# Performance work log

Measured on AMD Instinct MI355X. Metric: run time of the kernel, lower is better.

## Reference

```python
import jax, jax.numpy as jnp
import numpy as np

N, E = 50000, 800000          # nodes, edges
CUR, HID, OUT = 128, 128, 128  # cur_dim, hidden_dim, output_dim
NEG_SLOPE = 0.01               # F.leaky_relu default


def setup_inputs() -> dict:
    key = jax.random.key(0)
    ks = jax.random.split(key, 12)
    rn = lambda k, shp, s: jax.random.normal(k, shp, dtype=jnp.float32) * s
    s_c, s_h, s_o = 1.0 / np.sqrt(CUR), 1.0 / np.sqrt(HID), 1.0 / np.sqrt(OUT)
    return {
        "h": rn(ks[0], (N, CUR), 1.0),
        "x": rn(ks[1], (N, CUR), 1.0),
        "edge_index": jax.random.randint(ks[2], (2, E), 0, N, dtype=jnp.int32),
        "edge_weight": jax.random.uniform(ks[3], (E,), dtype=jnp.float32),
        # preprocessor_x: Linear(CUR, HID)
        "Wp": rn(ks[4], (HID, CUR), s_c), "bp": jnp.zeros((HID,), jnp.float32),
        # ChebConv(HID, OUT, K=2): two weight mats + bias
        "Wc0": rn(ks[5], (OUT, HID), s_h), "Wc1": rn(ks[6], (OUT, HID), s_h),
        "bc": jnp.zeros((OUT,), jnp.float32),
        # SAGEConv(HID, OUT): lin_rel (neighbors, with bias) + lin_root (self)
        "Wrel": rn(ks[7], (OUT, HID), s_h), "brel": jnp.zeros((OUT,), jnp.float32),
        "Wroot": rn(ks[8], (OUT, HID), s_h),
        # final Linear(OUT, OUT)
        "Wl": rn(ks[9], (OUT, OUT), s_o), "bl": jnp.zeros((OUT,), jnp.float32),
    }


def reference(h, x, edge_index, edge_weight, Wp, bp, Wc0, Wc1, bc,
              Wrel, brel, Wroot, Wl, bl):
    n = x.shape[0]
    src, dst = edge_index[0], edge_index[1]
    seg = lambda d, i: jax.ops.segment_sum(d, i, num_segments=n)

    his = x
    xh = x @ Wp.T + bp                               # [N, HID]

    # --- ChebConv, K=2, sym norm, lambda_max=2 => Lhat = -D^{-1/2} A D^{-1/2}
    deg = seg(edge_weight, src)                       # weighted degree
    dis = jnp.where(deg > 0, jax.lax.rsqrt(jnp.where(deg > 0, deg, 1.0)), 0.0)
    norm = -dis[src] * edge_weight * dis[dst]         # [E]
    Tx1 = seg(norm[:, None] * xh[src], dst)           # [N, HID]
    o1 = jax.nn.leaky_relu(xh @ Wc0.T + Tx1 @ Wc1.T + bc, NEG_SLOPE)

    # --- SAGEConv: mean of edge_weight-scaled neighbor feats + root transform
    msum = seg(edge_weight[:, None] * xh[src], dst)   # [N, HID]
    cnt = seg(jnp.ones_like(edge_weight), dst)        # in-degree
    mean = msum / jnp.maximum(cnt, 1.0)[:, None]
    o2 = jax.nn.leaky_relu(mean @ Wrel.T + brel + xh @ Wroot.T, NEG_SLOPE)

    o3 = (o1 + o2) @ Wl.T + bl
    return (his, o3)
```

## Files before the change

kernel.cpp:

```cpp
#include <hip/hip_runtime.h>

#define NN 50000
#define EE 800000
#define D  128
#define NCH 64
#define CH  12500
#define NR  8
#define RS  6250
#define KCB 512
#define XHB 782
#define CSB 196
#define PKB 384

typedef short short8 __attribute__((ext_vector_type(8)));
typedef float floatx4 __attribute__((ext_vector_type(4)));

__device__ __forceinline__ float leaky(float v) { return v > 0.f ? v : 0.01f * v; }

__device__ __forceinline__ unsigned short f2bf(float f) {
    unsigned int u = __float_as_uint(f);
    u = (u + 0x7fff + ((u >> 16) & 1)) >> 16;
    return (unsigned short)u;
}
__device__ __forceinline__ float bf2f(unsigned int h) {
    return __uint_as_float(h << 16);
}

__global__ __launch_bounds__(256) void k_pre(
    const float* __restrict__ Wp,  const float* __restrict__ Wc0,
    const float* __restrict__ Wc1, const float* __restrict__ Wrel,
    const float* __restrict__ Wroot, const float* __restrict__ Wl,
    unsigned short* __restrict__ Pall) {
    int gid = blockIdx.x * 256 + threadIdx.x;
    int mm = gid >> 14;
    int r = gid & 16383;
    int j  = r & 7;
    int l  = (r >> 3) & 63;
    int ct = (r >> 9) & 7;
    int kc = r >> 12;
    int n = ct * 16 + (l & 15);
    int k = kc * 32 + (l >> 4) * 8 + j;
    const float* W = mm == 0 ? Wp : mm == 1 ? Wc0 : mm == 2 ? Wc1
                   : mm == 3 ? Wrel : mm == 4 ? Wroot : Wl;
    Pall[gid] = f2bf(W[n * 128 + k]);
}

__global__ __launch_bounds__(256) void k_main(
    const int* __restrict__ src, const int* __restrict__ dst,
    const float* __restrict__ ew,
    int* __restrict__ counts,
    float* __restrict__ degp,
    unsigned short* __restrict__ rank,
    const float* __restrict__ x, const float* __restrict__ bp,
    unsigned short* __restrict__ xh16, float* __restrict__ his,
    const unsigned short* __restrict__ Pall) {
    __shared__ int   scnt[RS];
    __shared__ float sdeg[RS];
    int b = blockIdx.x;
    if (b < KCB) {
        int c = b & 63;
        int rge = b >> 6;
        int rlo = rge * RS;
        for (int i = threadIdx.x; i < RS; i += 256) { scnt[i] = 0; sdeg[i] = 0.f; }
        __syncthreads();
        int base = c * CH;
        for (int i0 = threadIdx.x * 4; i0 < CH; i0 += 1024) {
            int e = base + i0;
            int4   s4 = *(const int4*)(src + e);
            int4   d4 = *(const int4*)(dst + e);
            float4 w4 = *(const float4*)(ew + e);
            unsigned dr, sr;
            dr = (unsigned)(d4.x - rlo);
            if (dr < RS) rank[e]     = (unsigned short)atomicAdd(&scnt[dr], 1);
            sr = (unsigned)(s4.x - rlo);
            if (sr < RS) atomicAdd(&sdeg[sr], w4.x);
            dr = (unsigned)(d4.y - rlo);
            if (dr < RS) rank[e + 1] = (unsigned short)atomicAdd(&scnt[dr], 1);
            sr = (unsigned)(s4.y - rlo);
            if (sr < RS) atomicAdd(&sdeg[sr], w4.y);
            dr = (unsigned)(d4.z - rlo);
            if (dr < RS) rank[e + 2] = (unsigned short)atomicAdd(&scnt[dr], 1);
            sr = (unsigned)(s4.z - rlo);
            if (sr < RS) atomicAdd(&sdeg[sr], w4.z);
            dr = (unsigned)(d4.w - rlo);
            if (dr < RS) rank[e + 3] = (unsigned short)atomicAdd(&scnt[dr], 1);
            sr = (unsigned)(s4.w - rlo);
            if (sr < RS) atomicAdd(&sdeg[sr], w4.w);
        }
        __syncthreads();
        size_t ob = (size_t)c * NN + rlo;
        for (int i = threadIdx.x; i < RS; i += 256) {
            counts[ob + i] = scnt[i];
            degp[ob + i]   = sdeg[i];
        }
    } else {
        int bb = b - KCB;
        const unsigned short* Pp = Pall;
        int wave = threadIdx.x >> 6, l = threadIdx.x & 63;
        int n0 = bb * 64 + wave * 16;
        int m = l & 15, q = l >> 4;
        int nodeA = n0 + m;
        bool av = nodeA < NN;
        int na = av ? nodeA : 0;
        floatx4 acc[8];
#pragma unroll
        for (int ct = 0; ct < 8; ++ct) acc[ct] = (floatx4)(0.f);
#pragma unroll
        for (int kc = 0; kc < 4; ++kc) {
            const float* ap = x + (size_t)na * 128 + kc * 32 + q * 8;
            float4 f0 = av ? *(const float4*)ap       : make_float4(0, 0, 0, 0);
            float4 f1 = av ? *(const float4*)(ap + 4) : make_float4(0, 0, 0, 0);
            if (av) {
                float* hp = his + (size_t)nodeA * 128 + kc * 32 + q * 8;
                *(float4*)hp       = f0;
                *(float4*)(hp + 4) = f1;
            }
            short8 a;
            a[0] = f2bf(f0.x); a[1] = f2bf(f0.y); a[2] = f2bf(f0.z); a[3] = f2bf(f0.w);
            a[4] = f2bf(f1.x); a[5] = f2bf(f1.y); a[6] = f2bf(f1.z); a[7] = f2bf(f1.w);
#pragma unroll
            for (int ct = 0; ct < 8; ++ct) {
                short8 bfr = *(const short8*)(Pp + ((kc * 8 + ct) << 9) + l * 8);
                acc[ct] = __builtin_amdgcn_mfma_f32_16x16x32_bf16(a, bfr, acc[ct], 0, 0, 0);
            }
        }
#pragma unroll
        for (int ct = 0; ct < 8; ++ct) {
            int col = ct * 16 + m;
            float bias = bp[col];
#pragma unroll
            for (int r = 0; r < 4; ++r) {
                int node = n0 + q * 4 + r;
                if (node < NN) xh16[(size_t)node * 128 + col] = f2bf(acc[ct][r] + bias);
            }
        }
    }
}

__global__ __launch_bounds__(256) void k_colscan(int* __restrict__ counts,
                                                 const float* __restrict__ degp,
                                                 int* __restrict__ cntI,
                                                 float* __restrict__ deg,
                                                 int* __restrict__ blocksum) {
    __shared__ int ws4[4];
    int t = threadIdx.x;
    int n = blockIdx.x * 256 + t;
    int acc = 0; float dacc = 0.f;
    if (n < NN) {
#pragma unroll 8
        for (int c = 0; c < NCH; ++c) {
            size_t idx = (size_t)c * NN + n;
            int v = counts[idx];
            counts[idx] = acc;
            acc += v;
            dacc += degp[idx];
        }
        cntI[n] = acc;
        deg[n] = dacc;
    }
    int s = (n < NN) ? acc : 0;
#pragma unroll
    for (int off = 32; off > 0; off >>= 1) s += __shfl_down(s, off, 64);
    if ((t & 63) == 0) ws4[t >> 6] = s;
    __syncthreads();
    if (t == 0) blocksum[blockIdx.x] = ws4[0] + ws4[1] + ws4[2] + ws4[3];
}

__global__ __launch_bounds__(256) void k_scan_mid(const int* __restrict__ blocksum,
                                                  int* __restrict__ blockoff,
                                                  int* __restrict__ rowstart) {
    __shared__ int wtot[4];
    int t = threadIdx.x, lane = t & 63, wave = t >> 6;
    int v = (t < CSB) ? blocksum[t] : 0;
    int incl = v;
#pragma unroll
    for (int off = 1; off < 64; off <<= 1) {
        int u = __shfl_up(incl, off, 64);
        if (lane >= off) incl += u;
    }
    if (lane == 63) wtot[wave] = incl;
    __syncthreads();
    int wpre = 0;
    for (int w = 0; w < wave; ++w) wpre += wtot[w];
    incl += wpre;
    if (t < CSB) blockoff[t] = incl - v;
    if (t == 255) rowstart[NN] = incl;
}

__global__ __launch_bounds__(256) void k_scan_final(const int* __restrict__ cntI,
                                                    const int* __restrict__ blockoff,
                                                    int* __restrict__ rowstart) {
    __shared__ int wtot[4];
    int t = threadIdx.x, lane = t & 63, wave = t >> 6;
    int n = blockIdx.x * 256 + t;
    int v = (n < NN) ? cntI[n] : 0;
    int incl = v;
#pragma unroll
    for (int off = 1; off < 64; off <<= 1) {
        int u = __shfl_up(incl, off, 64);
        if (lane >= off) incl += u;
    }
    if (lane == 63) wtot[wave] = incl;
    __syncthreads();
    int wpre = 0;
    for (int w = 0; w < wave; ++w) wpre += wtot[w];
    incl += wpre;
    if (n < NN) rowstart[n] = blockoff[blockIdx.x] + incl - v;
}

__global__ __launch_bounds__(256) void k_bucket(const int* __restrict__ src,
                                                const int* __restrict__ dst,
                                                const float* __restrict__ ew,
                                                const float* __restrict__ deg,
                                                const int* __restrict__ rowstart,
                                                const int* __restrict__ chunkoff,
                                                const unsigned short* __restrict__ rank,
                                                int4* __restrict__ rec) {
    int e = blockIdx.x * blockDim.x + threadIdx.x;
    if (e >= EE) return;
    int s = src[e], d = dst[e];
    float w = ew[e];
    float degs = deg[s];
    float dis_s = degs > 0.f ? rsqrtf(degs) : 0.f;
    int c = e / CH;
    int pos = rowstart[d] + chunkoff[(size_t)c * NN + d] + (int)rank[e];
    int4 r;
    r.x = s;
    r.y = __float_as_int(w);
    r.z = __float_as_int(dis_s * w);
    r.w = 0;
    rec[pos] = r;
}

__global__ __launch_bounds__(256) void k_gather(const int* __restrict__ rowstart,
                                                const int4* __restrict__ rec,
                                                const float* __restrict__ deg,
                                                const unsigned short* __restrict__ xh16,
                                                unsigned int* __restrict__ tx16,
                                                unsigned int* __restrict__ mn16) {
    int wave = threadIdx.x >> 6, l = threadIdx.x & 63;
    int n = blockIdx.x * 4 + wave;
    if (n >= NN) return;
    int lo = rowstart[n], hi = rowstart[n + 1];
    float at0 = 0.f, at1 = 0.f, am0 = 0.f, am1 = 0.f;
    int e = lo;
    for (; e + 3 < hi; e += 4) {
        int4 r0 = rec[e], r1 = rec[e + 1], r2 = rec[e + 2], r3 = rec[e + 3];
        unsigned int v0 = *(const unsigned int*)(xh16 + (size_t)r0.x * 128 + l * 2);
        unsigned int v1 = *(const unsigned int*)(xh16 + (size_t)r1.x * 128 + l * 2);
        unsigned int v2 = *(const unsigned int*)(xh16 + (size_t)r2.x * 128 + l * 2);
        unsigned int v3 = *(const unsigned int*)(xh16 + (size_t)r3.x * 128 + l * 2);
        float w0 = __int_as_float(r0.y), u0 = __int_as_float(r0.z);
        float w1 = __int_as_float(r1.y), u1 = __int_as_float(r1.z);
        float w2 = __int_as_float(r2.y), u2 = __int_as_float(r2.z);
        float w3 = __int_as_float(r3.y), u3 = __int_as_float(r3.z);
        float a0 = bf2f(v0 & 0xffff), a1 = bf2f(v0 >> 16);
        float b0 = bf2f(v1 & 0xffff), b1 = bf2f(v1 >> 16);
        float c0 = bf2f(v2 & 0xffff), c1 = bf2f(v2 >> 16);
        float d0 = bf2f(v3 & 0xffff), d1 = bf2f(v3 >> 16);
        am0 = fmaf(w0, a0, am0); am1 = fmaf(w0, a1, am1);
        at0 = fmaf(u0, a0, at0); at1 = fmaf(u0, a1, at1);
        am0 = fmaf(w1, b0, am0); am1 = fmaf(w1, b1, am1);
        at0 = fmaf(u1, b0, at0); at1 = fmaf(u1, b1, at1);
        am0 = fmaf(w2, c0, am0); am1 = fmaf(w2, c1, am1);
        at0 = fmaf(u2, c0, at0); at1 = fmaf(u2, c1, at1);
        am0 = fmaf(w3, d0, am0); am1 = fmaf(w3, d1, am1);
        at0 = fmaf(u3, d0, at0); at1 = fmaf(u3, d1, at1);
    }
    for (; e < hi; ++e) {
        int4 r0 = rec[e];
        unsigned int v0 = *(const unsigned int*)(xh16 + (size_t)r0.x * 128 + l * 2);
        float w0 = __int_as_float(r0.y), u0 = __int_as_float(r0.z);
        float a0 = bf2f(v0 & 0xffff), a1 = bf2f(v0 >> 16);
        am0 = fmaf(w0, a0, am0); am1 = fmaf(w0, a1, am1);
        at0 = fmaf(u0, a0, at0); at1 = fmaf(u0, a1, at1);
    }
    float dd = deg[n];
    float dis_d = dd > 0.f ? rsqrtf(dd) : 0.f;
    int c = hi - lo;
    float ic = 1.f / (float)(c > 0 ? c : 1);
    unsigned int tpack = (unsigned int)f2bf(-dis_d * at0) |
                         ((unsigned int)f2bf(-dis_d * at1) << 16);
    unsigned int mpack = (unsigned int)f2bf(am0 * ic) |
                         ((unsigned int)f2bf(am1 * ic) << 16);
    tx16[(size_t)n * 64 + l] = tpack;
    mn16[(size_t)n * 64 + l] = mpack;
}

__global__ __launch_bounds__(256) void k_fused(const unsigned short* __restrict__ xh16,
                                               const unsigned short* __restrict__ tx16,
                                               const unsigned short* __restrict__ mn16,
                                               const unsigned short* __restrict__ Pall,
                                               const float* __restrict__ bc,
                                               const float* __restrict__ brel,
                                               const float* __restrict__ bl,
                                               float* __restrict__ out) {
    const unsigned short* Pc0  = Pall + 1 * 16384;
    const unsigned short* Pc1  = Pall + 2 * 16384;
    const unsigned short* Prel = Pall + 3 * 16384;
    const unsigned short* Proot= Pall + 4 * 16384;
    const unsigned short* Pl   = Pall + 5 * 16384;
    __shared__ __align__(16) unsigned short sS[4][16][136];
    int wave = threadIdx.x >> 6, l = threadIdx.x & 63;
    int n0 = blockIdx.x * 64 + wave * 16;
    int m = l & 15, q = l >> 4;
    int nodeA = n0 + m;
    bool av = nodeA < NN;
    size_t ra = (size_t)(av ? nodeA : 0) * 128 + q * 8;
    floatx4 acc1[8], acc2[8];
#pragma unroll
    for (int ct = 0; ct < 8; ++ct) { acc1[ct] = (floatx4)(0.f); acc2[ct] = (floatx4)(0.f); }
#pragma unroll
    for (int kc = 0; kc < 4; ++kc) {
        short8 a_xh = *(const short8*)(xh16 + ra + kc * 32);
        short8 a_tx = *(const short8*)(tx16 + ra + kc * 32);
        short8 a_mn = *(const short8*)(mn16 + ra + kc * 32);
#pragma unroll
        for (int ct = 0; ct < 8; ++ct) {
            int po = ((kc * 8 + ct) << 9) + l * 8;
            short8 b0 = *(const short8*)(Pc0 + po);
            short8 b1 = *(const short8*)(Pc1 + po);
            short8 b2 = *(const short8*)(Prel + po);
            short8 b3 = *(const short8*)(Proot + po);
            acc1[ct] = __builtin_amdgcn_mfma_f32_16x16x32_bf16(a_xh, b0, acc1[ct], 0, 0, 0);
            acc1[ct] = __builtin_amdgcn_mfma_f32_16x16x32_bf16(a_tx, b1, acc1[ct], 0, 0, 0);
            acc2[ct] = __builtin_amdgcn_mfma_f32_16x16x32_bf16(a_mn, b2, acc2[ct], 0, 0, 0);
            acc2[ct] = __builtin_amdgcn_mfma_f32_16x16x32_bf16(a_xh, b3, acc2[ct], 0, 0, 0);
        }
    }
#pragma unroll
    for (int ct = 0; ct < 8; ++ct) {
        int col = ct * 16 + m;
        float b1v = bc[col], b2v = brel[col];
#pragma unroll
        for (int r = 0; r < 4; ++r) {
            float u = leaky(acc1[ct][r] + b1v) + leaky(acc2[ct][r] + b2v);
            sS[wave][q * 4 + r][col] = f2bf(u);
        }
    }
    floatx4 acc3[8];
#pragma unroll
    for (int ct = 0; ct < 8; ++ct) acc3[ct] = (floatx4)(0.f);
#pragma unroll
    for (int kc = 0; kc < 4; ++kc) {
        short8 a_s = *(const short8*)&sS[wave][m][kc * 32 + q * 8];
#pragma unroll
        for (int ct = 0; ct < 8; ++ct) {
            short8 b = *(const short8*)(Pl + ((kc * 8 + ct) << 9) + l * 8);
            acc3[ct] = __builtin_amdgcn_mfma_f32_16x16x32_bf16(a_s, b, acc3[ct], 0, 0, 0);
        }
    }
#pragma unroll
    for (int ct = 0; ct < 8; ++ct) {
        int col = ct * 16 + m;
        float bv = bl[col];
#pragma unroll
        for (int r = 0; r < 4; ++r) {
            int node = n0 + q * 4 + r;
            if (node < NN) out[(size_t)node * 128 + col] = acc3[ct][r] + bv;
        }
    }
}

extern "C" void kernel_launch(void* const* d_in, const int* in_sizes, int n_in,
                              void* d_out, int out_size, void* d_ws, size_t ws_size,
                              hipStream_t stream) {
    const float* x    = (const float*)d_in[1];
    const int*   ei   = (const int*)d_in[2];
    const float* ew   = (const float*)d_in[3];
    const float* Wp   = (const float*)d_in[4];
    const float* bp   = (const float*)d_in[5];
    const float* Wc0  = (const float*)d_in[6];
    const float* Wc1  = (const float*)d_in[7];
    const float* bc   = (const float*)d_in[8];
    const float* Wrel = (const float*)d_in[9];
    const float* brel = (const float*)d_in[10];
    const float* Wroot= (const float*)d_in[11];
    const float* Wl   = (const float*)d_in[12];
    const float* bl   = (const float*)d_in[13];
    (void)in_sizes; (void)n_in; (void)out_size; (void)ws_size;
    float* out = (float*)d_out;

    unsigned short* xh16 = (unsigned short*)d_ws;
    unsigned short* tx16 = xh16 + (size_t)NN * 128;
    unsigned short* mn16 = tx16 + (size_t)NN * 128;
    unsigned short* Pall = mn16 + (size_t)NN * 128;
    int*   counts = (int*)(Pall + 6 * 16384);
    int4*  rec    = (int4*)(counts + (size_t)NCH * NN);
    float* degp   = (float*)rec;
    unsigned short* rank = (unsigned short*)(rec + EE);
    int*   rowstart = (int*)(rank + EE);
    int*   blocksum = rowstart + NN + 2;
    int*   blockoff = blocksum + CSB;
    int*   cntI   = blockoff + CSB;
    float* deg    = (float*)(cntI + NN);

    const int* srcI = ei;
    const int* dstI = ei + EE;

    k_pre<<<PKB, 256, 0, stream>>>(Wp, Wc0, Wc1, Wrel, Wroot, Wl, Pall);
    k_main<<<KCB + XHB, 256, 0, stream>>>(
        srcI, dstI, ew, counts, degp, rank, x, bp, xh16, out, Pall);
    k_colscan<<<CSB, 256, 0, stream>>>(counts, degp, cntI, deg, blocksum);
    k_scan_mid<<<1, 256, 0, stream>>>(blocksum, blockoff, rowstart);
    k_scan_final<<<CSB, 256, 0, stream>>>(cntI, blockoff, rowstart);
    k_bucket<<<(EE + 255) / 256, 256, 0, stream>>>(srcI, dstI, ew, deg, rowstart,
                                                   counts, rank, rec);
    k_gather<<<(NN + 3) / 4, 256, 0, stream>>>(rowstart, rec, deg, xh16,
                                               (unsigned int*)tx16, (unsigned int*)mn16);
    k_fused<<<(NN + 63) / 64, 256, 0, stream>>>(xh16, tx16, mn16, Pall,
                                                bc, brel, bl, out + (size_t)NN * 128);
}
```

Before: 269.9 us.

## Switch fused dense stage to 32x32x16 MFMA tiles with swizzled LDS

Moves the final fused GEMM kernel from 16x16x32 to 32x32x16 bf16 MFMA, so each wave handles 32 nodes and each block 128. The weight packing in k_pre is changed to the matching B-fragment layout for the five weight matrices this stage uses. The A fragments are preloaded into registers, and the intermediate tile in LDS uses an XOR swizzle to avoid bank conflicts. The aim is to halve how often weights are reloaded per node and to make the MFMA work denser, at the cost of more registers, which launch_bounds(256,2) caps.

```diff
diff --git a/kernel.cpp b/kernel.cpp
--- a/kernel.cpp
+++ b/kernel.cpp
@@ -11,9 +11,11 @@
 #define XHB 782
 #define CSB 196
 #define PKB 384
+#define FB  391
 
 typedef short short8 __attribute__((ext_vector_type(8)));
 typedef float floatx4 __attribute__((ext_vector_type(4)));
+typedef float floatx16 __attribute__((ext_vector_type(16)));
 
 __device__ __forceinline__ float leaky(float v) { return v > 0.f ? v : 0.01f * v; }
 
@@ -36,10 +38,18 @@
     int r = gid & 16383;
     int j  = r & 7;
     int l  = (r >> 3) & 63;
-    int ct = (r >> 9) & 7;
-    int kc = r >> 12;
-    int n = ct * 16 + (l & 15);
-    int k = kc * 32 + (l >> 4) * 8 + j;
+    int n, k;
+    if (mm == 0) {
+        int ct = (r >> 9) & 7;
+        int kc = r >> 12;
+        n = ct * 16 + (l & 15);
+        k = kc * 32 + (l >> 4) * 8 + j;
+    } else {
+        int ct = (r >> 9) & 3;
+        int kc = (r >> 11) & 7;
+        n = ct * 32 + (l & 31);
+        k = kc * 16 + (l >> 5) * 8 + j;
+    }
     const float* W = mm == 0 ? Wp : mm == 1 ? Wc0 : mm == 2 ? Wc1
                    : mm == 3 ? Wrel : mm == 4 ? Wroot : Wl;
     Pall[gid] = f2bf(W[n * 128 + k]);
@@ -287,7 +297,7 @@
     mn16[(size_t)n * 64 + l] = mpack;
 }
 
-__global__ __launch_bounds__(256) void k_fused(const unsigned short* __restrict__ xh16,
+__global__ __launch_bounds__(256, 2) void k_fused(const unsigned short* __restrict__ xh16,
                                                const unsigned short* __restrict__ tx16,
                                                const unsigned short* __restrict__ mn16,
                                                const unsigned short* __restrict__ Pall,
@@ -300,64 +310,66 @@
     const unsigned short* Prel = Pall + 3 * 16384;
     const unsigned short* Proot= Pall + 4 * 16384;
     const unsigned short* Pl   = Pall + 5 * 16384;
-    __shared__ __align__(16) unsigned short sS[4][16][136];
-    int wave = threadIdx.x >> 6, l = threadIdx.x & 63;
-    int n0 = blockIdx.x * 64 + wave * 16;
-    int m = l & 15, q = l >> 4;
-    int nodeA = n0 + m;
-    bool av = nodeA < NN;
-    size_t ra = (size_t)(av ? nodeA : 0) * 128 + q * 8;
-    floatx4 acc1[8], acc2[8];
-#pragma unroll
-    for (int ct = 0; ct < 8; ++ct) { acc1[ct] = (floatx4)(0.f); acc2[ct] = (floatx4)(0.f); }
-#pragma unroll
-    for (int kc = 0; kc < 4; ++kc) {
-        short8 a_xh = *(const short8*)(xh16 + ra + kc * 32);
-        short8 a_tx = *(const short8*)(tx16 + ra + kc * 32);
-        short8 a_mn = *(const short8*)(mn16 + ra + kc * 32);
-#pragma unroll
-        for (int ct = 0; ct < 8; ++ct) {
-            int po = ((kc * 8 + ct) << 9) + l * 8;
+    __shared__ __align__(16) unsigned short sS[4][32][128];
+    int w = threadIdx.x >> 6, l = threadIdx.x & 63;
+    int n0 = blockIdx.x * 128 + w * 32;
+    int row = l & 31, half = l >> 5;
+    int node = n0 + row;
+    bool av = node < NN;
+    size_t ra = (size_t)(av ? node : 0) * 128 + half * 8;
+    short8 Axh[8], Atx[8], Amn[8];
+#pragma unroll
+    for (int kc = 0; kc < 8; ++kc) {
+        Axh[kc] = *(const short8*)(xh16 + ra + kc * 16);
+        Atx[kc] = *(const short8*)(tx16 + ra + kc * 16);
+        Amn[kc] = *(const short8*)(mn16 + ra + kc * 16);
+    }
+#pragma unroll
+    for (int ct = 0; ct < 4; ++ct) {
+        floatx16 acc1 = (floatx16)(0.f), acc2 = (floatx16)(0.f);
+#pragma unroll
+        for (int kc = 0; kc < 8; ++kc) {
+            int po = ((kc * 4 + ct) << 9) + l * 8;
             short8 b0 = *(const short8*)(Pc0 + po);
             short8 b1 = *(const short8*)(Pc1 + po);
             short8 b2 = *(const short8*)(Prel + po);
             short8 b3 = *(const short8*)(Proot + po);
-            acc1[ct] = __builtin_amdgcn_mfma_f32_16x16x32_bf16(a_xh, b0, acc1[ct], 0, 0, 0);
-            acc1[ct] = __builtin_amdgcn_mfma_f32_16x16x32_bf16(a_tx, b1, acc1[ct], 0, 0, 0);
-            acc2[ct] = __builtin_amdgcn_mfma_f32_16x16x32_bf16(a_mn, b2, acc2[ct], 0, 0, 0);
-            acc2[ct] = __builtin_amdgcn_mfma_f32_16x16x32_bf16(a_xh, b3, acc2[ct], 0, 0, 0);
-        }
-    }
-#pragma unroll
-    for (int ct = 0; ct < 8; ++ct) {
-        int col = ct * 16 + m;
+            acc1 = __builtin_amdgcn_mfma_f32_32x32x16_bf16(Axh[kc], b0, acc1, 0, 0, 0);
+            acc1 = __builtin_amdgcn_mfma_f32_32x32x16_bf16(Atx[kc], b1, acc1, 0, 0, 0);
+            acc2 = __builtin_amdgcn_mfma_f32_32x32x16_bf16(Amn[kc], b2, acc2, 0, 0, 0);
+            acc2 = __builtin_amdgcn_mfma_f32_32x32x16_bf16(Axh[kc], b3, acc2, 0, 0, 0);
+        }
+        int col = ct * 32 + row;
         float b1v = bc[col], b2v = brel[col];
 #pragma unroll
-        for (int r = 0; r < 4; ++r) {
-            float u = leaky(acc1[ct][r] + b1v) + leaky(acc2[ct][r] + b2v);
-            sS[wave][q * 4 + r][col] = f2bf(u);
-        }
-    }
-    floatx4 acc3[8];
-#pragma unroll
-    for (int ct = 0; ct < 8; ++ct) acc3[ct] = (floatx4)(0.f);
-#pragma unroll
-    for (int kc = 0; kc < 4; ++kc) {
-        short8 a_s = *(const short8*)&sS[wave][m][kc * 32 + q * 8];
-#pragma unroll
-        for (int ct = 0; ct < 8; ++ct) {
-            short8 b = *(const short8*)(Pl + ((kc * 8 + ct) << 9) + l * 8);
-            acc3[ct] = __builtin_amdgcn_mfma_f32_16x16x32_bf16(a_s, b, acc3[ct], 0, 0, 0);
-        }
-    }
-#pragma unroll
-    for (int ct = 0; ct < 8; ++ct) {
-        int col = ct * 16 + m;
+        for (int r = 0; r < 16; ++r) {
+            int rr = (r & 3) + 8 * (r >> 2) + 4 * half;
+            float u = leaky(acc1[r] + b1v) + leaky(acc2[r] + b2v);
+            int sw = ((((col >> 3) ^ rr) & 15) << 3) | (col & 7);
+            sS[w][rr][sw] = f2bf(u);
+        }
+    }
+    short8 As[8];
+#pragma unroll
+    for (int kc = 0; kc < 8; ++kc) {
+        int g = (kc * 2 + half) ^ (row & 15);
+        As[kc] = *(const short8*)&sS[w][row][g << 3];
+    }
+#pragma unroll
+    for (int ct = 0; ct < 4; ++ct) {
+        floatx16 acc3 = (floatx16)(0.f);
+#pragma unroll
+        for (int kc = 0; kc < 8; ++kc) {
+            short8 b = *(const short8*)(Pl + ((kc * 4 + ct) << 9) + l * 8);
+            acc3 = __builtin_amdgcn_mfma_f32_32x32x16_bf16(As[kc], b, acc3, 0, 0, 0);
+        }
+        int col = ct * 32 + row;
         float bv = bl[col];
 #pragma unroll
-        for (int r = 0; r < 4; ++r) {
-            int node = n0 + q * 4 + r;
-            if (node < NN) out[(size_t)node * 128 + col] = acc3[ct][r] + bv;
+        for (int r = 0; r < 16; ++r) {
+            int rr = (r & 3) + 8 * (r >> 2) + 4 * half;
+            int nd = n0 + rr;
+            if (nd < NN) out[(size_t)nd * 128 + col] = acc3[r] + bv;
         }
     }
 }
@@ -408,6 +420,6 @@
                                                    counts, rank, rec);
     k_gather<<<(NN + 3) / 4, 256, 0, stream>>>(rowstart, rec, deg, xh16,
                                                (unsigned int*)tx16, (unsigned int*)mn16);
-    k_fused<<<(NN + 63) / 64, 256, 0, stream>>>(xh16, tx16, mn16, Pall,
-                                                bc, brel, bl, out + (size_t)NN * 128);
-}
+    k_fused<<<FB, 256, 0, stream>>>(xh16, tx16, mn16, Pall,
+                                    bc, brel, bl, out + (size_t)NN * 128);
+}
```

Result: no change. 266.0 us (-1.4%).
